# Performance work log

Hardware: AMD Instinct MI355X
Metric: run time of the kernel (lower is better)

## Reference

```python
import jax, jax.numpy as jnp
import numpy as np

B, S, HID, NH, W = 4, 4096, 768, 12, 128  # batch, seq, hidden, heads, one-sided window
D = HID // NH


def setup_inputs() -> dict:
    key = jax.random.key(0)
    ks = jax.random.split(key, 4)
    sc = 0.02
    return {
        "hidden_states": jax.random.normal(ks[0], (B, S, HID), jnp.float32),
        "Wq": jax.random.normal(ks[1], (HID, HID), jnp.float32) * sc,
        "bq": jnp.zeros((HID,), jnp.float32),
        "Wk": jax.random.normal(ks[2], (HID, HID), jnp.float32) * sc,
        "bk": jnp.zeros((HID,), jnp.float32),
        "Wv": jax.random.normal(ks[3], (HID, HID), jnp.float32) * sc,
        "bv": jnp.zeros((HID,), jnp.float32),
    }


def _heads(x):
    # [B,S,HID] -> [B*NH, S, D]  (matches transpose_for_scores)
    return x.reshape(B, S, NH, D).transpose(0, 2, 1, 3).reshape(B * NH, S, D)


def _windows(x, w):
    # x: [BH, S, D] -> overlapping key/value windows [BH, S//w, 3w, D]
    xp = jnp.pad(x, ((0, 0), (w, w), (0, 0)))
    xc = xp.reshape(x.shape[0], S // w + 2, w, D)
    return jnp.concatenate([xc[:, :-2], xc[:, 1:-1], xc[:, 2:]], axis=2)


def sliding_window_attention(q, k, v, w):
    # q,k,v: [BH, S, D]; banded attention with 2w+1 diagonals, edges masked -inf
    BH = q.shape[0]
    C = S // w
    qc = (q * (1.0 / np.sqrt(D))).reshape(BH, C, w, D)
    kw = _windows(k, w)                                   # [BH,C,3w,D]
    scores_full = jnp.einsum('bcxd,bcyd->bcxy', qc, kw)   # [BH,C,w,3w]
    x = jnp.arange(w)
    off = jnp.arange(2 * w + 1)
    idx = x[:, None] + off[None, :]                       # [w, 2w+1] diag gather index
    scores = jnp.take_along_axis(scores_full, idx[None, None], axis=-1)  # [BH,C,w,2w+1]
    # mask key positions outside [0, S) (== _mask_invalid_locations)
    qpos = jnp.arange(C)[:, None, None] * w + x[:, None]  # [C,w,1]
    kpos = qpos + off[None, None, :] - w                  # [C,w,2w+1]
    valid = (kpos >= 0) & (kpos < S)
    scores = jnp.where(valid[None], scores, -jnp.inf)
    probs = jax.nn.softmax(scores, axis=-1)
    # scatter banded probs back to chunked [w, 3w] layout, then probs @ value windows
    pw = jnp.zeros((BH, C, w, 3 * w), probs.dtype).at[:, :, x[:, None], idx].set(probs)
    vw = _windows(v, w)                                   # [BH,C,3w,D]
    ctx = jnp.einsum('bcxy,bcyd->bcxd', pw, vw)           # [BH,C,w,D]
    return ctx.reshape(BH, S, D)


def reference(hidden_states, Wq, bq, Wk, bk, Wv, bv):
    q = _heads(hidden_states @ Wq.T + bq)
    k = _heads(hidden_states @ Wk.T + bk)
    v = _heads(hidden_states @ Wv.T + bv)
    ctx = sliding_window_attention(q, k, v, W)            # [B*NH, S, D]
    out = ctx.reshape(B, NH, S, D).transpose(0, 2, 1, 3).reshape(B, S, HID)
    return out
```

## Files before the change

kernel.cpp:

```cpp
#include <hip/hip_runtime.h>

#define BQ 4
#define SQ 4096
#define HIDN 768
#define NH 12
#define DH 64
#define BH (BQ * NH)
#define WIN 128
#define MROWS (BQ * SQ)
#define NCOLS (3 * HIDN)
#define KDIM HIDN
#define BHD_ELEMS (BH * SQ * DH)

using bfrag  = __attribute__((ext_vector_type(8))) short;
using f32x4  = __attribute__((ext_vector_type(4))) float;
using f32x16 = __attribute__((ext_vector_type(16))) float;
using us8    = __attribute__((ext_vector_type(8))) unsigned short;

__device__ __forceinline__ unsigned short f2bf(float f) {
  union { float f; unsigned u; } x; x.f = f;
  unsigned r = x.u + 0x7fffu + ((x.u >> 16) & 1u);
  return (unsigned short)(r >> 16);
}
__device__ __forceinline__ unsigned f2bf2(float lo, float hi) {
  return (unsigned)f2bf(lo) | ((unsigned)f2bf(hi) << 16);
}
__device__ __forceinline__ unsigned cvtpk(float lo, float hi) {
  unsigned u;
  asm("v_cvt_pk_bf16_f32 %0, %1, %2" : "=v"(u) : "v"(lo), "v"(hi));
  return u;
}

__device__ __forceinline__ void gload16(const void* g, void* l) {
  __builtin_amdgcn_global_load_lds(
      (const __attribute__((address_space(1))) unsigned int*)g,
      (__attribute__((address_space(3))) unsigned int*)l, 16, 0, 0);
}

__global__ __launch_bounds__(256) void wconv_kernel(
    const float* __restrict__ Wq, const float* __restrict__ Wk,
    const float* __restrict__ Wv, unsigned short* __restrict__ wb)
{
  int i = blockIdx.x * 256 + threadIdx.x;
  int g = i * 4;
  if (g >= NCOLS * KDIM) return;
  int n = g / KDIM, k = g - n * KDIM;
  int wsel = n / HIDN, nl = n - wsel * HIDN;
  const float* W = (wsel == 0) ? Wq : (wsel == 1) ? Wk : Wv;
  float4 v = *reinterpret_cast<const float4*>(&W[nl * KDIM + k]);
  ushort4 p;
  p.x = f2bf(v.x); p.y = f2bf(v.y); p.z = f2bf(v.z); p.w = f2bf(v.w);
  *reinterpret_cast<ushort4*>(&wb[g]) = p;
}

__global__ __launch_bounds__(256) void hconv_kernel(
    const float* __restrict__ hid, unsigned short* __restrict__ hb)
{
  const int N8 = MROWS * KDIM / 8;
  for (int idx = blockIdx.x * 256 + threadIdx.x; idx < N8; idx += gridDim.x * 256) {
    const float4* src = reinterpret_cast<const float4*>(hid) + (size_t)idx * 2;
    float4 a = src[0], b = src[1];
    uint4 o;
    o.x = f2bf2(a.x, a.y); o.y = f2bf2(a.z, a.w);
    o.z = f2bf2(b.x, b.y); o.w = f2bf2(b.z, b.w);
    *reinterpret_cast<uint4*>(&hb[(size_t)idx * 8]) = o;
  }
}

#define BM 128
#define BN 128
#define BKK 64

__global__ __launch_bounds__(256) void proj_kernel(
    const unsigned short* __restrict__ hb,
    const unsigned short* __restrict__ wb,
    const float* __restrict__ bq, const float* __restrict__ bk,
    const float* __restrict__ bv,
    unsigned short* __restrict__ qb, unsigned short* __restrict__ kb,
    unsigned short* __restrict__ vb)
{
  __shared__ unsigned short As[BM][BKK];
  __shared__ unsigned short Bs[BN][BKK];

  const int t = threadIdx.x;
  const int id = blockIdx.x;
  const int swz = (id & 7) * (NCOLS * MROWS / (BM * BN) / 8) + (id >> 3);
  const int bx = swz % (NCOLS / BN);
  const int by = swz / (NCOLS / BN);
  const int m0 = by * BM;
  const int n0 = bx * BN;
  const int wsel = bx / 6;
  const float* bias = (wsel == 0) ? bq : (wsel == 1) ? bk : bv;
  const int nloc0 = n0 - wsel * HIDN;

  const int lane = t & 63;
  const int w = t >> 6;
  const int wm = w >> 1, wn = w & 1;
  const int fr = lane & 15, fq = lane >> 4;
  const int xsw = (fr & 7) << 3;

  const int srow = w * 32 + (lane >> 3);
  const int scol = ((lane & 7) * 8) ^ ((lane >> 3) << 3);
  const unsigned short* gA = &hb[(size_t)(m0 + srow) * KDIM + scol];
  const unsigned short* gB = &wb[(size_t)(n0 + srow) * KDIM + scol];

  f32x4 acc[4][4] = {};

  for (int kt = 0; kt < KDIM / BKK; ++kt) {
    const int k0 = kt * BKK;
    __syncthreads();
    #pragma unroll
    for (int i = 0; i < 4; ++i) {
      gload16(gA + k0 + (size_t)(i * 8) * KDIM, &As[w * 32 + i * 8][0]);
      gload16(gB + k0 + (size_t)(i * 8) * KDIM, &Bs[w * 32 + i * 8][0]);
    }
    __syncthreads();
    #pragma unroll
    for (int kk = 0; kk < 2; ++kk) {
      bfrag a[4], b[4];
      #pragma unroll
      for (int i = 0; i < 4; ++i)
        a[i] = *reinterpret_cast<const bfrag*>(&As[wm * 64 + i * 16 + fr][(kk * 32 + fq * 8) ^ xsw]);
      #pragma unroll
      for (int j = 0; j < 4; ++j)
        b[j] = *reinterpret_cast<const bfrag*>(&Bs[wn * 64 + j * 16 + fr][(kk * 32 + fq * 8) ^ xsw]);
      #pragma unroll
      for (int i = 0; i < 4; ++i)
        #pragma unroll
        for (int j = 0; j < 4; ++j)
          acc[i][j] = __builtin_amdgcn_mfma_f32_16x16x32_bf16(b[j], a[i], acc[i][j], 0, 0, 0);
    }
  }

  unsigned short* outb = (wsel == 0) ? qb : (wsel == 1) ? kb : vb;
  const float qscale = (wsel == 0) ? 0.125f * 1.44269504088896f : 1.0f;
  const int b_ = m0 >> 12;
  #pragma unroll
  for (int j = 0; j < 4; ++j) {
    int nl = nloc0 + wn * 64 + j * 16 + fq * 4;
    int h = nl >> 6, d0 = nl & 63;
    float4 bs4 = *reinterpret_cast<const float4*>(&bias[nl]);
    unsigned short* obase = outb + (size_t)(b_ * NH + h) * SQ * DH + d0;
    #pragma unroll
    for (int i = 0; i < 4; ++i) {
      int m = m0 + wm * 64 + i * 16 + fr;
      int srow_ = m & (SQ - 1);
      f32x4 v = acc[i][j];
      uint2 pk;
      pk.x = f2bf2((v[0] + bs4.x) * qscale, (v[1] + bs4.y) * qscale);
      pk.y = f2bf2((v[2] + bs4.z) * qscale, (v[3] + bs4.w) * qscale);
      *reinterpret_cast<uint2*>(&obase[(size_t)srow_ * DH]) = pk;
    }
  }
}

#define VLD 392
#define THR 11.6f

__global__ __launch_bounds__(256, 3) void attn_kernel(
    const unsigned short* __restrict__ qb,
    const unsigned short* __restrict__ kb,
    const unsigned short* __restrict__ vb,
    float* __restrict__ out)
{
  __shared__ unsigned short Vt[DH][VLD];

  const int c = blockIdx.x;
  const int bh = blockIdx.y;
  const int t = threadIdx.x;
  const int lane = t & 63;
  const int w = t >> 6;
  const int b_ = bh / NH, hd = bh - b_ * NH;
  const int qi = lane & 31, h = lane >> 5;

  const unsigned short* Qbh = qb + bh * (SQ * DH);
  const unsigned short* Kbh = kb + bh * (SQ * DH);
  const unsigned short* Vbh = vb + bh * (SQ * DH);

  const int kstart = c * 128 - WIN;

  for (int it = t; it < 48 * 16; it += 256) {
    int dg = it & 15, kg = it >> 4;
    int kr = kstart + kg * 8;
    ushort4 va[8];
    #pragma unroll
    for (int rr = 0; rr < 8; ++rr) {
      int k = kr + rr;
      int kc = k < 0 ? 0 : (k > SQ - 1 ? SQ - 1 : k);
      va[rr] = *reinterpret_cast<const ushort4*>(&Vbh[(size_t)kc * DH + dg * 4]);
    }
    #pragma unroll
    for (int j = 0; j < 4; ++j) {
      us8 row;
      #pragma unroll
      for (int i = 0; i < 8; ++i)
        row[i] = reinterpret_cast<const unsigned short*>(&va[i])[j];
      *reinterpret_cast<us8*>(&Vt[dg * 4 + j][kg * 8]) = row;
    }
  }
  __syncthreads();

  const int q0w = c * 128 + w * 32;
  const int q = q0w + qi;
  const int kw = q0w - WIN;
  bfrag qf[4];
  #pragma unroll
  for (int kk = 0; kk < 4; ++kk)
    qf[kk] = *reinterpret_cast<const bfrag*>(&Qbh[(size_t)q * DH + kk * 16 + h * 8]);

  const int lo = (-q > -WIN) ? -q : -WIN;
  const int hi = (SQ - 1 - q < WIN) ? (SQ - 1 - q) : WIN;
  const int hq = 4 * h - qi;
  const bool edge = (c == 0) || (c == 31);

  f32x16 c0 = {}, c1 = {};
  float m = -3e38f, ls = 0.f;

  for (int kt = 0; kt < 9; ++kt) {
    int krow = kw + kt * 32 + qi;
    int kc = krow < 0 ? 0 : (krow > SQ - 1 ? SQ - 1 : krow);
    bfrag kf[4];
    #pragma unroll
    for (int kk = 0; kk < 4; ++kk)
      kf[kk] = *reinterpret_cast<const bfrag*>(&Kbh[(size_t)kc * DH + kk * 16 + h * 8]);

    f32x16 D = {};
    __builtin_amdgcn_s_setprio(1);
    #pragma unroll
    for (int kk = 0; kk < 4; ++kk)
      D = __builtin_amdgcn_mfma_f32_32x32x16_bf16(kf[kk], qf[kk], D, 0, 0, 0);
    __builtin_amdgcn_s_setprio(0);

    if (edge || kt == 0 || kt == 8) {
      #pragma unroll
      for (int r = 0; r < 16; ++r) {
        int klocal = (r & 3) + 8 * (r >> 2);
        int dk = kt * 32 + klocal - WIN + hq;
        if (dk < lo || dk > hi) D[r] = -1e30f;
      }
    }

    float pm = D[0];
    #pragma unroll
    for (int r = 1; r < 16; ++r) pm = fmaxf(pm, D[r]);
    pm = fmaxf(pm, __shfl_xor(pm, 32));

    if (!__all(pm <= m + THR)) {
      float mn = fmaxf(m, pm);
      float al = __builtin_amdgcn_exp2f(m - mn);
      #pragma unroll
      for (int r = 0; r < 16; ++r) {
        float av = __shfl(al, (r & 3) + 8 * (r >> 2) + 4 * h);
        c0[r] *= av; c1[r] *= av;
      }
      ls *= al;
      m = mn;
    }

    float p[16];
    float sum = 0.f;
    #pragma unroll
    for (int r = 0; r < 16; ++r) {
      p[r] = __builtin_amdgcn_exp2f(D[r] - m);
      sum += p[r];
    }
    ls += sum;

    unsigned U[8];
    #pragma unroll
    for (int g = 0; g < 8; ++g) U[g] = cvtpk(p[2 * g], p[2 * g + 1]);

    unsigned f0[4], f1[4];
    {
      unsigned x, y, xs, ys;
      x = U[0]; y = U[2]; xs = __shfl_xor(x, 32); ys = __shfl_xor(y, 32);
      f0[0] = h ? ys : x;  f0[2] = h ? y : xs;
      x = U[1]; y = U[3]; xs = __shfl_xor(x, 32); ys = __shfl_xor(y, 32);
      f0[1] = h ? ys : x;  f0[3] = h ? y : xs;
      x = U[4]; y = U[6]; xs = __shfl_xor(x, 32); ys = __shfl_xor(y, 32);
      f1[0] = h ? ys : x;  f1[2] = h ? y : xs;
      x = U[5]; y = U[7]; xs = __shfl_xor(x, 32); ys = __shfl_xor(y, 32);
      f1[1] = h ? ys : x;  f1[3] = h ? y : xs;
    }

    const int colbase = w * 32 + kt * 32;
    bfrag paA, paB;
    {
      uint4 ua = {f0[0], f0[1], f0[2], f0[3]};
      uint4 ub = {f1[0], f1[1], f1[2], f1[3]};
      paA = *reinterpret_cast<bfrag*>(&ua);
      paB = *reinterpret_cast<bfrag*>(&ub);
    }
    bfrag v00 = *reinterpret_cast<const bfrag*>(&Vt[qi][colbase + h * 8]);
    bfrag v01 = *reinterpret_cast<const bfrag*>(&Vt[32 + qi][colbase + h * 8]);
    bfrag v10 = *reinterpret_cast<const bfrag*>(&Vt[qi][colbase + 16 + h * 8]);
    bfrag v11 = *reinterpret_cast<const bfrag*>(&Vt[32 + qi][colbase + 16 + h * 8]);
    __builtin_amdgcn_s_setprio(1);
    c0 = __builtin_amdgcn_mfma_f32_32x32x16_bf16(paA, v00, c0, 0, 0, 0);
    c1 = __builtin_amdgcn_mfma_f32_32x32x16_bf16(paA, v01, c1, 0, 0, 0);
    c0 = __builtin_amdgcn_mfma_f32_32x32x16_bf16(paB, v10, c0, 0, 0, 0);
    c1 = __builtin_amdgcn_mfma_f32_32x32x16_bf16(paB, v11, c1, 0, 0, 0);
    __builtin_amdgcn_s_setprio(0);
  }

  float lt = ls + __shfl_xor(ls, 32);
  float rinv = 1.0f / lt;
  #pragma unroll
  for (int r = 0; r < 16; ++r) {
    int qrow = (r & 3) + 8 * (r >> 2) + 4 * h;
    float rv = __shfl(rinv, qrow);
    size_t obase = (size_t)(b_ * SQ + q0w + qrow) * HIDN + hd * DH;
    out[obase + qi] = c0[r] * rv;
    out[obase + 32 + qi] = c1[r] * rv;
  }
}

extern "C" void kernel_launch(void* const* d_in, const int* in_sizes, int n_in,
                              void* d_out, int out_size, void* d_ws, size_t ws_size,
                              hipStream_t stream) {
  const float* hid = (const float*)d_in[0];
  const float* Wq  = (const float*)d_in[1];
  const float* bq  = (const float*)d_in[2];
  const float* Wk  = (const float*)d_in[3];
  const float* bk  = (const float*)d_in[4];
  const float* Wv  = (const float*)d_in[5];
  const float* bv  = (const float*)d_in[6];
  float* out = (float*)d_out;

  unsigned short* qb = (unsigned short*)d_ws;
  unsigned short* kb = qb + BHD_ELEMS;
  unsigned short* vb = kb + BHD_ELEMS;
  unsigned short* wb = vb + BHD_ELEMS;
  unsigned short* hb = wb + NCOLS * KDIM;

  int nconv = (NCOLS * KDIM / 4 + 255) / 256;
  wconv_kernel<<<dim3(nconv), dim3(256), 0, stream>>>(Wq, Wk, Wv, wb);
  hconv_kernel<<<dim3(2048), dim3(256), 0, stream>>>(hid, hb);

  dim3 g1(NCOLS * MROWS / (BM * BN));
  proj_kernel<<<g1, dim3(256), 0, stream>>>(hb, wb, bq, bk, bv, qb, kb, vb);

  dim3 g2(SQ / 128, BH);
  attn_kernel<<<g2, dim3(256), 0, stream>>>(qb, kb, vb, out);
}
```

Before: 150.7 us.

## Multi-stage LDS pipeline for QKV projection GEMM with smaller K tiles

Rewrites the projection GEMM main loop as a 4-slot LDS ring buffer with K-tile 32, issuing async global-to-LDS loads three tiles ahead. Each iteration uses a partial vmcnt wait and a single barrier instead of two full syncs. It also raises wave priority around the MFMA block. The goal is to hide global load latency behind matrix math. The cost is a packed two-rows-per-LDS-row swizzled layout, a circular wraparound prefetch that issues redundant loads at the end, and hand-tuned waitcnt counts that could be fragile.

```diff
diff --git a/kernel.cpp b/kernel.cpp
--- a/kernel.cpp
+++ b/kernel.cpp
@@ -67,9 +67,10 @@
   }
 }
 
-#define BM 128
-#define BN 128
-#define BKK 64
+#define PBM 128
+#define PBN 128
+#define PBK 32
+#define NKT (KDIM / PBK)
 
 __global__ __launch_bounds__(256) void proj_kernel(
     const unsigned short* __restrict__ hb,
@@ -79,16 +80,16 @@
     unsigned short* __restrict__ qb, unsigned short* __restrict__ kb,
     unsigned short* __restrict__ vb)
 {
-  __shared__ unsigned short As[BM][BKK];
-  __shared__ unsigned short Bs[BN][BKK];
+  __shared__ unsigned short As[4][64][64];
+  __shared__ unsigned short Bs[4][64][64];
 
   const int t = threadIdx.x;
   const int id = blockIdx.x;
-  const int swz = (id & 7) * (NCOLS * MROWS / (BM * BN) / 8) + (id >> 3);
-  const int bx = swz % (NCOLS / BN);
-  const int by = swz / (NCOLS / BN);
-  const int m0 = by * BM;
-  const int n0 = bx * BN;
+  const int swz = (id & 7) * (NCOLS * MROWS / (PBM * PBN) / 8) + (id >> 3);
+  const int bx = swz % (NCOLS / PBN);
+  const int by = swz / (NCOLS / PBN);
+  const int m0 = by * PBM;
+  const int n0 = bx * PBN;
   const int wsel = bx / 6;
   const float* bias = (wsel == 0) ? bq : (wsel == 1) ? bk : bv;
   const int nloc0 = n0 - wsel * HIDN;
@@ -97,38 +98,71 @@
   const int w = t >> 6;
   const int wm = w >> 1, wn = w & 1;
   const int fr = lane & 15, fq = lane >> 4;
-  const int xsw = (fr & 7) << 3;
-
-  const int srow = w * 32 + (lane >> 3);
-  const int scol = ((lane & 7) * 8) ^ ((lane >> 3) << 3);
-  const unsigned short* gA = &hb[(size_t)(m0 + srow) * KDIM + scol];
-  const unsigned short* gB = &wb[(size_t)(n0 + srow) * KDIM + scol];
+
+  const int e_lane = ((lane & 7) * 8) ^ ((lane >> 3) << 3);
+  const int sub = e_lane >> 5;
+  const int kk_lane = e_lane & 31;
+  const int lr0 = w * 16 + (lane >> 3);
+  const unsigned short* gA0 = &hb[(size_t)(m0 + lr0 * 2 + sub) * KDIM + kk_lane];
+  const unsigned short* gA1 = &hb[(size_t)(m0 + (lr0 + 8) * 2 + sub) * KDIM + kk_lane];
+  const unsigned short* gB0 = &wb[(size_t)(n0 + lr0 * 2 + sub) * KDIM + kk_lane];
+  const unsigned short* gB1 = &wb[(size_t)(n0 + (lr0 + 8) * 2 + sub) * KDIM + kk_lane];
+
+  int oA[4], oB[4];
+  #pragma unroll
+  for (int i = 0; i < 4; ++i) {
+    int rA = wm * 64 + i * 16 + fr;
+    int lrA = rA >> 1;
+    oA[i] = lrA * 64 + (((rA & 1) * 32 + fq * 8) ^ ((lrA & 7) << 3));
+    int rB = wn * 64 + i * 16 + fr;
+    int lrB = rB >> 1;
+    oB[i] = lrB * 64 + (((rB & 1) * 32 + fq * 8) ^ ((lrB & 7) << 3));
+  }
+  const unsigned short* Afl = &As[0][0][0];
+  const unsigned short* Bfl = &Bs[0][0][0];
 
   f32x4 acc[4][4] = {};
 
-  for (int kt = 0; kt < KDIM / BKK; ++kt) {
-    const int k0 = kt * BKK;
-    __syncthreads();
-    #pragma unroll
-    for (int i = 0; i < 4; ++i) {
-      gload16(gA + k0 + (size_t)(i * 8) * KDIM, &As[w * 32 + i * 8][0]);
-      gload16(gB + k0 + (size_t)(i * 8) * KDIM, &Bs[w * 32 + i * 8][0]);
-    }
-    __syncthreads();
-    #pragma unroll
-    for (int kk = 0; kk < 2; ++kk) {
+  #pragma unroll
+  for (int pt = 0; pt < 3; ++pt) {
+    const int k0 = pt * PBK;
+    gload16(gA0 + k0, &As[pt][w * 16][0]);
+    gload16(gA1 + k0, &As[pt][w * 16 + 8][0]);
+    gload16(gB0 + k0, &Bs[pt][w * 16][0]);
+    gload16(gB1 + k0, &Bs[pt][w * 16 + 8][0]);
+  }
+  asm volatile("s_waitcnt vmcnt(8)" ::: "memory");
+  __builtin_amdgcn_s_barrier();
+  __builtin_amdgcn_sched_barrier(0);
+
+  for (int tb = 0; tb < NKT; tb += 4) {
+    #pragma unroll
+    for (int u = 0; u < 4; ++u) {
+      const int kt = tb + u;
+      int kst = kt + 3; if (kst >= NKT) kst -= NKT;
+      const int slw = (kt + 3) & 3;
+      const int k0s = kst * PBK;
+      gload16(gA0 + k0s, &As[slw][w * 16][0]);
+      gload16(gA1 + k0s, &As[slw][w * 16 + 8][0]);
+      gload16(gB0 + k0s, &Bs[slw][w * 16][0]);
+      gload16(gB1 + k0s, &Bs[slw][w * 16 + 8][0]);
+      const int sbase = (kt & 3) * 64 * 64;
       bfrag a[4], b[4];
       #pragma unroll
-      for (int i = 0; i < 4; ++i)
-        a[i] = *reinterpret_cast<const bfrag*>(&As[wm * 64 + i * 16 + fr][(kk * 32 + fq * 8) ^ xsw]);
-      #pragma unroll
-      for (int j = 0; j < 4; ++j)
-        b[j] = *reinterpret_cast<const bfrag*>(&Bs[wn * 64 + j * 16 + fr][(kk * 32 + fq * 8) ^ xsw]);
+      for (int i = 0; i < 4; ++i) {
+        a[i] = *reinterpret_cast<const bfrag*>(&Afl[sbase + oA[i]]);
+        b[i] = *reinterpret_cast<const bfrag*>(&Bfl[sbase + oB[i]]);
+      }
+      __builtin_amdgcn_s_setprio(1);
       #pragma unroll
       for (int i = 0; i < 4; ++i)
         #pragma unroll
         for (int j = 0; j < 4; ++j)
           acc[i][j] = __builtin_amdgcn_mfma_f32_16x16x32_bf16(b[j], a[i], acc[i][j], 0, 0, 0);
+      __builtin_amdgcn_s_setprio(0);
+      asm volatile("s_waitcnt vmcnt(8)" ::: "memory");
+      __builtin_amdgcn_s_barrier();
+      __builtin_amdgcn_sched_barrier(0);
     }
   }
 
@@ -337,7 +371,7 @@
   wconv_kernel<<<dim3(nconv), dim3(256), 0, stream>>>(Wq, Wk, Wv, wb);
   hconv_kernel<<<dim3(2048), dim3(256), 0, stream>>>(hid, hb);
 
-  dim3 g1(NCOLS * MROWS / (BM * BN));
+  dim3 g1(NCOLS * MROWS / (PBM * PBN));
   proj_kernel<<<g1, dim3(256), 0, stream>>>(hb, wb, bq, bk, bv, qb, kb, vb);
 
   dim3 g2(SQ / 128, BH);
```

Result: slower. 169.8 us (+12.7%).
